# Kernel tuning notes

Hardware: AMD Instinct MI355X
Metric: run time of the kernel (lower is better)

The kernel has to match this reference:

```python
import jax, jax.numpy as jnp
import numpy as np

N_RULES = 64  # R
OUT_PER_RULE = 64  # O, fc out = R*O = 4096


def setup_inputs() -> dict:
    key = jax.random.key(0)
    k1, k2, k3, k4 = jax.random.split(key, 4)
    S, D_IN = 8192, 1024
    RO = N_RULES * OUT_PER_RULE
    X = jax.random.normal(k1, (S, D_IN), dtype=jnp.float32)
    # torch.nn.Linear-style weight [out, in] and bias [out]
    W = jax.random.normal(k2, (RO, D_IN), dtype=jnp.float32) * (1.0 / np.sqrt(D_IN))
    b = jax.random.normal(k3, (RO,), dtype=jnp.float32) * 0.01
    # rule firing strengths (computed under no_grad in the original)
    lambdas = jax.random.uniform(k4, (S, N_RULES), dtype=jnp.float32)
    return {"X": X, "W": W, "b": b, "lambdas": lambdas}


def reference(X, W, b, lambdas):
    # fc + sigmoid: [S, R*O]
    H = jax.nn.sigmoid(X @ W.T + b)
    S = H.shape[0]
    # apply_rule_strength: block-diagonal lambda_eye @ H^T is exactly a
    # rule-weighted sum over the R consecutive O-sized blocks of H.
    Hr = H.reshape(S, N_RULES, OUT_PER_RULE)  # [S, R, O]
    Y = jnp.einsum("sr,sro->so", lambdas, Hr)  # [S, O]
    return Y
```

## Files before the change

kernel.cpp:

```cpp
#include <hip/hip_runtime.h>

#define S_DIM 8192
#define K_DIM 1024
#define RO_DIM 4096
#define O_DIM 64
#define SO (S_DIM * O_DIM)
#define NSLICE 16

typedef __attribute__((ext_vector_type(8))) __bf16 bf16x8;
typedef __attribute__((ext_vector_type(4))) float floatx4;
typedef __attribute__((ext_vector_type(4))) unsigned short ushx4;
typedef __attribute__((ext_vector_type(8))) unsigned short ushx8;

__device__ inline unsigned short f2bf(float f) {
  unsigned u = __builtin_bit_cast(unsigned, f);
  u += 0x7fff + ((u >> 16) & 1);
  return (unsigned short)(u >> 16);
}
__device__ inline float bf2f(unsigned short h) {
  unsigned u = ((unsigned)h) << 16;
  return __builtin_bit_cast(float, u);
}

__global__ __launch_bounds__(256) void cast_kernel(const float* __restrict__ X,
                                                   const float* __restrict__ W,
                                                   unsigned short* __restrict__ Xb,
                                                   unsigned short* __restrict__ Wb) {
  const int NX4 = (S_DIM * K_DIM) / 4;
#pragma unroll
  for (int i = 0; i < 4; ++i) {
    int g = blockIdx.x * 1024 + i * 256 + threadIdx.x;
    float4 v;
    unsigned short* dst;
    if (g < NX4) {
      v = ((const float4*)X)[g];
      dst = Xb + (size_t)g * 4;
    } else {
      int j = g - NX4;
      v = ((const float4*)W)[j];
      dst = Wb + (size_t)j * 4;
    }
    ushx4 o;
    o.x = f2bf(v.x); o.y = f2bf(v.y); o.z = f2bf(v.z); o.w = f2bf(v.w);
    *(ushx4*)dst = o;
  }
}


template <int MB, int NB>
__device__ __forceinline__ void mfmaq(floatx4 (&acc)[8][4], const bf16x8 (&afr)[4][2],
                                      const bf16x8 (&bfr)[4][2]) {
  __builtin_amdgcn_s_setprio(1);
#pragma unroll
  for (int m = 0; m < 4; ++m)
#pragma unroll
    for (int n = 0; n < 2; ++n) {
      acc[MB + m][NB + n] = __builtin_amdgcn_mfma_f32_16x16x32_bf16(
          afr[m][0], bfr[NB + n][0], acc[MB + m][NB + n], 0, 0, 0);
      acc[MB + m][NB + n] = __builtin_amdgcn_mfma_f32_16x16x32_bf16(
          afr[m][1], bfr[NB + n][1], acc[MB + m][NB + n], 0, 0, 0);
    }
  __builtin_amdgcn_s_setprio(0);
}

#define BAR() __builtin_amdgcn_s_barrier()
#define LGKM0() asm volatile("s_waitcnt lgkmcnt(0)" ::: "memory")
#define SB0() __builtin_amdgcn_sched_barrier(0)

__global__ __launch_bounds__(512, 2) void gemm_kernel(const unsigned short* __restrict__ Xb,
                                                      const unsigned short* __restrict__ Wb,
                                                      const float* __restrict__ bias,
                                                      const float* __restrict__ lam,
                                                      unsigned short* __restrict__ partial) {
  __shared__ __align__(16) unsigned char smem[135168];
  unsigned short* sm = (unsigned short*)smem;
  float* lamsh = (float*)(smem + 131072);

  const int t = threadIdx.x;
  const int lane = t & 63;
  const int w = t >> 6;
  const int wm = w >> 2;
  const int wn = w & 3;
  const int quad = lane >> 4;
  const int l16 = lane & 15;

  int id = blockIdx.y * 16 + blockIdx.x;
  int x = id & 7;
  int j = id >> 3;
  const int bx = 2 * x + (j & 1);
  const int by = j >> 1;
  const int gm0 = by * 256;
  const int gn0 = bx * 256;

  const int rowt = t >> 3;
  const int gcc = (t & 7) ^ (rowt & 7);
  const size_t goff = (size_t)rowt * K_DIM + (size_t)gcc * 8;
  const unsigned short* Abase = Xb + (size_t)gm0 * K_DIM;
  const unsigned short* Bbase = Wb + (size_t)gn0 * K_DIM;

  auto STAGE = [&](const unsigned short* gbase, int half, int ktile, int slotOff) {
#pragma unroll
    for (int jj = 0; jj < 2; ++jj) {
      const unsigned short* src =
          gbase + (size_t)(half * 128 + jj * 64) * K_DIM + ktile * 64 + goff;
      __builtin_amdgcn_global_load_lds(
          (const __attribute__((address_space(1))) void*)src,
          (__attribute__((address_space(3))) void*)(sm + slotOff + jj * 4096 + t * 8),
          16, 0, 0);
    }
  };

  STAGE(Abase, 0, 0, 0);
  STAGE(Abase, 1, 0, 8192);
  STAGE(Bbase, 0, 0, 16384);
  STAGE(Bbase, 1, 0, 24576);
  STAGE(Bbase, 0, 1, 32768 + 16384);
  STAGE(Bbase, 1, 1, 32768 + 24576);
  STAGE(Abase, 0, 1, 32768 + 0);

  {
    int i = t;
    lamsh[i] = lam[(size_t)(gm0 + (i >> 2)) * 64 + bx * 4 + (i & 3)];
    i = t + 512;
    lamsh[i] = lam[(size_t)(gm0 + (i >> 2)) * 64 + bx * 4 + (i & 3)];
  }
  asm volatile("s_waitcnt vmcnt(6)" ::: "memory");
  BAR();

  floatx4 acc[8][4];
#pragma unroll
  for (int ni = 0; ni < 4; ++ni) {
    float bv = bias[gn0 + wn * 64 + ni * 16 + l16];
#pragma unroll
    for (int mi = 0; mi < 8; ++mi) acc[mi][ni] = (floatx4){bv, bv, bv, bv};
  }

  const int cA0 = ((quad) ^ (l16 & 7)) * 8;
  const int cA1 = ((4 + quad) ^ (l16 & 7)) * 8;

  for (int kt = 0; kt < 16; ++kt) {
    const int b = kt & 1;
    const unsigned short* As = sm + b * 32768 + wm * 8192 + l16 * 64;
    const unsigned short* Bs = sm + b * 32768 + 16384 + wn * 4096 + l16 * 64;
    const int bufN = (b ^ 1) * 32768;
    const int bufC = b * 32768;

    bf16x8 afr[4][2], bfr[4][2];

#pragma unroll
    for (int m = 0; m < 4; ++m) {
      afr[m][0] = *(const bf16x8*)(As + m * 1024 + cA0);
      afr[m][1] = *(const bf16x8*)(As + m * 1024 + cA1);
    }
#pragma unroll
    for (int n = 0; n < 2; ++n) {
      bfr[n][0] = *(const bf16x8*)(Bs + n * 1024 + cA0);
      bfr[n][1] = *(const bf16x8*)(Bs + n * 1024 + cA1);
    }
    if (kt < 15) STAGE(Abase, 1, kt + 1, bufN + 8192);
    BAR();
    LGKM0();
    SB0();
    mfmaq<0, 0>(acc, afr, bfr);
    BAR();

#pragma unroll
    for (int n = 2; n < 4; ++n) {
      bfr[n][0] = *(const bf16x8*)(Bs + n * 1024 + cA0);
      bfr[n][1] = *(const bf16x8*)(Bs + n * 1024 + cA1);
    }
    BAR();
    LGKM0();
    SB0();
    mfmaq<0, 2>(acc, afr, bfr);
    BAR();

#pragma unroll
    for (int m = 0; m < 4; ++m) {
      afr[m][0] = *(const bf16x8*)(As + (4 + m) * 1024 + cA0);
      afr[m][1] = *(const bf16x8*)(As + (4 + m) * 1024 + cA1);
    }
    if (kt < 14) STAGE(Bbase, 0, kt + 2, bufC + 16384);
    BAR();
    LGKM0();
    SB0();
    mfmaq<4, 0>(acc, afr, bfr);
    BAR();

    if (kt < 14) {
      STAGE(Bbase, 1, kt + 2, bufC + 24576);
      STAGE(Abase, 0, kt + 2, bufC + 0);
    }
    SB0();
    mfmaq<4, 2>(acc, afr, bfr);
    SB0();
    if (kt < 14) {
      asm volatile("s_waitcnt vmcnt(6)" ::: "memory");
    } else if (kt == 14) {
      asm volatile("s_waitcnt vmcnt(0)" ::: "memory");
    }
    BAR();
  }

  __syncthreads();
  {
    unsigned short* yreg = sm + wn * 16384;
#pragma unroll
    for (int mi = 0; mi < 8; ++mi) {
#pragma unroll
      for (int r = 0; r < 4; ++r) {
        int row = wm * 128 + mi * 16 + quad * 4 + r;
        float lamv = lamsh[row * 4 + wn];
#pragma unroll
        for (int ni = 0; ni < 4; ++ni) {
          float sg = 1.f / (1.f + __expf(-acc[mi][ni][r]));
          yreg[row * 64 + ((ni ^ quad) * 16) + l16] = f2bf(lamv * sg);
        }
      }
    }
  }
  __syncthreads();
  {
    unsigned short* pb = partial + (size_t)bx * SO + (size_t)gm0 * 64;
#pragma unroll
    for (int g = 0; g < 4; ++g) {
      int idx = g * 4096 + t * 8;
      int row = idx >> 6;
      int c = idx & 63;
      int phys = row * 64 + ((((c >> 4) ^ ((row >> 2) & 3))) << 4) + (c & 15);
      float s[8];
#pragma unroll
      for (int jj = 0; jj < 8; ++jj) s[jj] = 0.f;
#pragma unroll
      for (int q = 0; q < 4; ++q) {
        ushx8 v = *(const ushx8*)(sm + q * 16384 + phys);
#pragma unroll
        for (int jj = 0; jj < 8; ++jj) s[jj] += bf2f(v[jj]);
      }
      ushx8 o;
#pragma unroll
      for (int jj = 0; jj < 8; ++jj) o[jj] = f2bf(s[jj]);
      *(ushx8*)(pb + idx) = o;
    }
  }
}

__global__ __launch_bounds__(256) void reduce_kernel(const unsigned short* __restrict__ partial,
                                                     float* __restrict__ Y) {
  int i4 = blockIdx.x * 256 + threadIdx.x;
  float s0 = 0.f, s1 = 0.f, s2 = 0.f, s3 = 0.f;
#pragma unroll
  for (int c = 0; c < NSLICE; ++c) {
    ushx4 v = ((const ushx4*)(partial + (size_t)c * SO))[i4];
    s0 += bf2f(v.x); s1 += bf2f(v.y); s2 += bf2f(v.z); s3 += bf2f(v.w);
  }
  ((float4*)Y)[i4] = (float4){s0, s1, s2, s3};
}

extern "C" void kernel_launch(void* const* d_in, const int* in_sizes, int n_in,
                              void* d_out, int out_size, void* d_ws, size_t ws_size,
                              hipStream_t stream) {
  const float* X = (const float*)d_in[0];
  const float* W = (const float*)d_in[1];
  const float* b = (const float*)d_in[2];
  const float* lam = (const float*)d_in[3];
  float* Y = (float*)d_out;

  unsigned short* Xb = (unsigned short*)d_ws;
  unsigned short* Wb = Xb + (size_t)S_DIM * K_DIM;
  unsigned short* partial = Wb + (size_t)RO_DIM * K_DIM;

  int nCast = ((S_DIM + RO_DIM) * K_DIM / 4) / 1024;
  cast_kernel<<<nCast, 256, 0, stream>>>(X, W, Xb, Wb);

  dim3 g(RO_DIM / 256, S_DIM / 256);
  gemm_kernel<<<g, 512, 0, stream>>>(Xb, Wb, b, lam, partial);

  reduce_kernel<<<SO / 1024, 256, 0, stream>>>(partial, Y);
}
```

Baseline: 167.3 us.

## Fuse cast, GEMM, and reduce into one cooperative persistent kernel

Replaces the three launches (bf16 cast, tiled GEMM with sigmoid and lambda epilogue, slice reduce) with one cooperative kernel of 256 blocks. The stages are separated by grid-wide syncs, and each block handles two M tiles in sequence. The aim is to remove per-launch overhead and the inter-kernel gaps. In exchange it adds two grid barriers, and the 256 resident blocks (2 per CU) may get less latency hiding and tail balancing than the original 512-block GEMM grid.

New measurement: 435.8 us. 160% more time.

```diff
diff --git a/kernel.cpp b/kernel.cpp
--- a/kernel.cpp
+++ b/kernel.cpp
@@ -1,4 +1,7 @@
 #include <hip/hip_runtime.h>
+#include <hip/hip_cooperative_groups.h>
+
+namespace cg = cooperative_groups;
 
 #define S_DIM 8192
 #define K_DIM 1024
@@ -22,31 +25,6 @@
   return __builtin_bit_cast(float, u);
 }
 
-__global__ __launch_bounds__(256) void cast_kernel(const float* __restrict__ X,
-                                                   const float* __restrict__ W,
-                                                   unsigned short* __restrict__ Xb,
-                                                   unsigned short* __restrict__ Wb) {
-  const int NX4 = (S_DIM * K_DIM) / 4;
-#pragma unroll
-  for (int i = 0; i < 4; ++i) {
-    int g = blockIdx.x * 1024 + i * 256 + threadIdx.x;
-    float4 v;
-    unsigned short* dst;
-    if (g < NX4) {
-      v = ((const float4*)X)[g];
-      dst = Xb + (size_t)g * 4;
-    } else {
-      int j = g - NX4;
-      v = ((const float4*)W)[j];
-      dst = Wb + (size_t)j * 4;
-    }
-    ushx4 o;
-    o.x = f2bf(v.x); o.y = f2bf(v.y); o.z = f2bf(v.z); o.w = f2bf(v.w);
-    *(ushx4*)dst = o;
-  }
-}
-
-
 template <int MB, int NB>
 __device__ __forceinline__ void mfmaq(floatx4 (&acc)[8][4], const bf16x8 (&afr)[4][2],
                                       const bf16x8 (&bfr)[4][2]) {
@@ -67,16 +45,46 @@
 #define LGKM0() asm volatile("s_waitcnt lgkmcnt(0)" ::: "memory")
 #define SB0() __builtin_amdgcn_sched_barrier(0)
 
-__global__ __launch_bounds__(512, 2) void gemm_kernel(const unsigned short* __restrict__ Xb,
-                                                      const unsigned short* __restrict__ Wb,
-                                                      const float* __restrict__ bias,
-                                                      const float* __restrict__ lam,
-                                                      unsigned short* __restrict__ partial) {
+__global__ __launch_bounds__(512, 2) void fused_kernel(const float* __restrict__ X,
+                                                       const float* __restrict__ W,
+                                                       const float* __restrict__ bias,
+                                                       const float* __restrict__ lam,
+                                                       unsigned short* __restrict__ Xb,
+                                                       unsigned short* __restrict__ Wb,
+                                                       unsigned short* __restrict__ partial,
+                                                       float* __restrict__ Y) {
   __shared__ __align__(16) unsigned char smem[135168];
   unsigned short* sm = (unsigned short*)smem;
   float* lamsh = (float*)(smem + 131072);
 
+  cg::grid_group grid = cg::this_grid();
+
   const int t = threadIdx.x;
+
+  {
+    const int NX4 = (S_DIM * K_DIM) / 4;
+    const int NT4 = NX4 + (RO_DIM * K_DIM) / 4;
+    int g = blockIdx.x * 512 + t;
+#pragma unroll 4
+    for (int it = 0; it < 24; ++it, g += 131072) {
+      float4 v;
+      unsigned short* dst;
+      if (g < NX4) {
+        v = ((const float4*)X)[g];
+        dst = Xb + (size_t)g * 4;
+      } else {
+        int jx = g - NX4;
+        v = ((const float4*)W)[jx];
+        dst = Wb + (size_t)jx * 4;
+      }
+      ushx4 o;
+      o.x = f2bf(v.x); o.y = f2bf(v.y); o.z = f2bf(v.z); o.w = f2bf(v.w);
+      *(ushx4*)dst = o;
+    }
+  }
+  __threadfence();
+  grid.sync();
+
   const int lane = t & 63;
   const int w = t >> 6;
   const int wm = w >> 2;
@@ -84,177 +92,185 @@
   const int quad = lane >> 4;
   const int l16 = lane & 15;
 
-  int id = blockIdx.y * 16 + blockIdx.x;
-  int x = id & 7;
-  int j = id >> 3;
+  const int id = blockIdx.x;
+  const int x = id & 7;
+  const int j = id >> 3;
   const int bx = 2 * x + (j & 1);
-  const int by = j >> 1;
-  const int gm0 = by * 256;
+  const int by0 = j >> 1;
   const int gn0 = bx * 256;
 
   const int rowt = t >> 3;
   const int gcc = (t & 7) ^ (rowt & 7);
   const size_t goff = (size_t)rowt * K_DIM + (size_t)gcc * 8;
-  const unsigned short* Abase = Xb + (size_t)gm0 * K_DIM;
   const unsigned short* Bbase = Wb + (size_t)gn0 * K_DIM;
-
-  auto STAGE = [&](const unsigned short* gbase, int half, int ktile, int slotOff) {
-#pragma unroll
-    for (int jj = 0; jj < 2; ++jj) {
-      const unsigned short* src =
-          gbase + (size_t)(half * 128 + jj * 64) * K_DIM + ktile * 64 + goff;
-      __builtin_amdgcn_global_load_lds(
-          (const __attribute__((address_space(1))) void*)src,
-          (__attribute__((address_space(3))) void*)(sm + slotOff + jj * 4096 + t * 8),
-          16, 0, 0);
-    }
-  };
-
-  STAGE(Abase, 0, 0, 0);
-  STAGE(Abase, 1, 0, 8192);
-  STAGE(Bbase, 0, 0, 16384);
-  STAGE(Bbase, 1, 0, 24576);
-  STAGE(Bbase, 0, 1, 32768 + 16384);
-  STAGE(Bbase, 1, 1, 32768 + 24576);
-  STAGE(Abase, 0, 1, 32768 + 0);
-
-  {
-    int i = t;
-    lamsh[i] = lam[(size_t)(gm0 + (i >> 2)) * 64 + bx * 4 + (i & 3)];
-    i = t + 512;
-    lamsh[i] = lam[(size_t)(gm0 + (i >> 2)) * 64 + bx * 4 + (i & 3)];
-  }
-  asm volatile("s_waitcnt vmcnt(6)" ::: "memory");
-  BAR();
-
-  floatx4 acc[8][4];
-#pragma unroll
-  for (int ni = 0; ni < 4; ++ni) {
-    float bv = bias[gn0 + wn * 64 + ni * 16 + l16];
-#pragma unroll
-    for (int mi = 0; mi < 8; ++mi) acc[mi][ni] = (floatx4){bv, bv, bv, bv};
-  }
 
   const int cA0 = ((quad) ^ (l16 & 7)) * 8;
   const int cA1 = ((4 + quad) ^ (l16 & 7)) * 8;
 
-  for (int kt = 0; kt < 16; ++kt) {
-    const int b = kt & 1;
-    const unsigned short* As = sm + b * 32768 + wm * 8192 + l16 * 64;
-    const unsigned short* Bs = sm + b * 32768 + 16384 + wn * 4096 + l16 * 64;
-    const int bufN = (b ^ 1) * 32768;
-    const int bufC = b * 32768;
-
-    bf16x8 afr[4][2], bfr[4][2];
-
-#pragma unroll
-    for (int m = 0; m < 4; ++m) {
-      afr[m][0] = *(const bf16x8*)(As + m * 1024 + cA0);
-      afr[m][1] = *(const bf16x8*)(As + m * 1024 + cA1);
-    }
-#pragma unroll
-    for (int n = 0; n < 2; ++n) {
-      bfr[n][0] = *(const bf16x8*)(Bs + n * 1024 + cA0);
-      bfr[n][1] = *(const bf16x8*)(Bs + n * 1024 + cA1);
-    }
-    if (kt < 15) STAGE(Abase, 1, kt + 1, bufN + 8192);
+  for (int rep = 0; rep < 2; ++rep) {
+    const int by = by0 + rep * 16;
+    const int gm0 = by * 256;
+    const unsigned short* Abase = Xb + (size_t)gm0 * K_DIM;
+
+    auto STAGE = [&](const unsigned short* gbase, int half, int ktile, int slotOff) {
+#pragma unroll
+      for (int jj = 0; jj < 2; ++jj) {
+        const unsigned short* src =
+            gbase + (size_t)(half * 128 + jj * 64) * K_DIM + ktile * 64 + goff;
+        __builtin_amdgcn_global_load_lds(
+            (const __attribute__((address_space(1))) void*)src,
+            (__attribute__((address_space(3))) void*)(sm + slotOff + jj * 4096 + t * 8),
+            16, 0, 0);
+      }
+    };
+
+    __syncthreads();
+
+    STAGE(Abase, 0, 0, 0);
+    STAGE(Abase, 1, 0, 8192);
+    STAGE(Bbase, 0, 0, 16384);
+    STAGE(Bbase, 1, 0, 24576);
+    STAGE(Bbase, 0, 1, 32768 + 16384);
+    STAGE(Bbase, 1, 1, 32768 + 24576);
+    STAGE(Abase, 0, 1, 32768 + 0);
+
+    {
+      int i = t;
+      lamsh[i] = lam[(size_t)(gm0 + (i >> 2)) * 64 + bx * 4 + (i & 3)];
+      i = t + 512;
+      lamsh[i] = lam[(size_t)(gm0 + (i >> 2)) * 64 + bx * 4 + (i & 3)];
+    }
+    asm volatile("s_waitcnt vmcnt(6)" ::: "memory");
     BAR();
-    LGKM0();
-    SB0();
-    mfmaq<0, 0>(acc, afr, bfr);
-    BAR();
-
-#pragma unroll
-    for (int n = 2; n < 4; ++n) {
-      bfr[n][0] = *(const bf16x8*)(Bs + n * 1024 + cA0);
-      bfr[n][1] = *(const bf16x8*)(Bs + n * 1024 + cA1);
-    }
-    BAR();
-    LGKM0();
-    SB0();
-    mfmaq<0, 2>(acc, afr, bfr);
-    BAR();
-
-#pragma unroll
-    for (int m = 0; m < 4; ++m) {
-      afr[m][0] = *(const bf16x8*)(As + (4 + m) * 1024 + cA0);
-      afr[m][1] = *(const bf16x8*)(As + (4 + m) * 1024 + cA1);
-    }
-    if (kt < 14) STAGE(Bbase, 0, kt + 2, bufC + 16384);
-    BAR();
-    LGKM0();
-    SB0();
-    mfmaq<4, 0>(acc, afr, bfr);
-    BAR();
-
-    if (kt < 14) {
-      STAGE(Bbase, 1, kt + 2, bufC + 24576);
-      STAGE(Abase, 0, kt + 2, bufC + 0);
-    }
-    SB0();
-    mfmaq<4, 2>(acc, afr, bfr);
-    SB0();
-    if (kt < 14) {
-      asm volatile("s_waitcnt vmcnt(6)" ::: "memory");
-    } else if (kt == 14) {
-      asm volatile("s_waitcnt vmcnt(0)" ::: "memory");
-    }
-    BAR();
+
+    floatx4 acc[8][4];
+#pragma unroll
+    for (int ni = 0; ni < 4; ++ni) {
+      float bv = bias[gn0 + wn * 64 + ni * 16 + l16];
+#pragma unroll
+      for (int mi = 0; mi < 8; ++mi) acc[mi][ni] = (floatx4){bv, bv, bv, bv};
+    }
+
+    for (int kt = 0; kt < 16; ++kt) {
+      const int b = kt & 1;
+      const unsigned short* As = sm + b * 32768 + wm * 8192 + l16 * 64;
+      const unsigned short* Bs = sm + b * 32768 + 16384 + wn * 4096 + l16 * 64;
+      const int bufN = (b ^ 1) * 32768;
+      const int bufC = b * 32768;
+
+      bf16x8 afr[4][2], bfr[4][2];
+
+#pragma unroll
+      for (int m = 0; m < 4; ++m) {
+        afr[m][0] = *(const bf16x8*)(As + m * 1024 + cA0);
+        afr[m][1] = *(const bf16x8*)(As + m * 1024 + cA1);
+      }
+#pragma unroll
+      for (int n = 0; n < 2; ++n) {
+        bfr[n][0] = *(const bf16x8*)(Bs + n * 1024 + cA0);
+        bfr[n][1] = *(const bf16x8*)(Bs + n * 1024 + cA1);
+      }
+      if (kt < 15) STAGE(Abase, 1, kt + 1, bufN + 8192);
+      BAR();
+      LGKM0();
+      SB0();
+      mfmaq<0, 0>(acc, afr, bfr);
+      BAR();
+
+#pragma unroll
+      for (int n = 2; n < 4; ++n) {
+        bfr[n][0] = *(const bf16x8*)(Bs + n * 1024 + cA0);
+        bfr[n][1] = *(const bf16x8*)(Bs + n * 1024 + cA1);
+      }
+      BAR();
+      LGKM0();
+      SB0();
+      mfmaq<0, 2>(acc, afr, bfr);
+      BAR();
+
+#pragma unroll
+      for (int m = 0; m < 4; ++m) {
+        afr[m][0] = *(const bf16x8*)(As + (4 + m) * 1024 + cA0);
+        afr[m][1] = *(const bf16x8*)(As + (4 + m) * 1024 + cA1);
+      }
+      if (kt < 14) STAGE(Bbase, 0, kt + 2, bufC + 16384);
+      BAR();
+      LGKM0();
+      SB0();
+      mfmaq<4, 0>(acc, afr, bfr);
+      BAR();
+
+      if (kt < 14) {
+        STAGE(Bbase, 1, kt + 2, bufC + 24576);
+        STAGE(Abase, 0, kt + 2, bufC + 0);
+      }
+      SB0();
+      mfmaq<4, 2>(acc, afr, bfr);
+      SB0();
+      if (kt < 14) {
+        asm volatile("s_waitcnt vmcnt(6)" ::: "memory");
+      } else if (kt == 14) {
+        asm volatile("s_waitcnt vmcnt(0)" ::: "memory");
+      }
+      BAR();
+    }
+
+    __syncthreads();
+    {
+      unsigned short* yreg = sm + wn * 16384;
+#pragma unroll
+      for (int mi = 0; mi < 8; ++mi) {
+#pragma unroll
+        for (int r = 0; r < 4; ++r) {
+          int row = wm * 128 + mi * 16 + quad * 4 + r;
+          float lamv = lamsh[row * 4 + wn];
+#pragma unroll
+          for (int ni = 0; ni < 4; ++ni) {
+            float sg = 1.f / (1.f + __expf(-acc[mi][ni][r]));
+            yreg[row * 64 + ((ni ^ quad) * 16) + l16] = f2bf(lamv * sg);
+          }
+        }
+      }
+    }
+    __syncthreads();
+    {
+      unsigned short* pb = partial + (size_t)bx * SO + (size_t)gm0 * 64;
+#pragma unroll
+      for (int g = 0; g < 4; ++g) {
+        int idx = g * 4096 + t * 8;
+        int row = idx >> 6;
+        int c = idx & 63;
+        int phys = row * 64 + ((((c >> 4) ^ ((row >> 2) & 3))) << 4) + (c & 15);
+        float s[8];
+#pragma unroll
+        for (int jj = 0; jj < 8; ++jj) s[jj] = 0.f;
+#pragma unroll
+        for (int q = 0; q < 4; ++q) {
+          ushx8 v = *(const ushx8*)(sm + q * 16384 + phys);
+#pragma unroll
+          for (int jj = 0; jj < 8; ++jj) s[jj] += bf2f(v[jj]);
+        }
+        ushx8 o;
+#pragma unroll
+        for (int jj = 0; jj < 8; ++jj) o[jj] = f2bf(s[jj]);
+        *(ushx8*)(pb + idx) = o;
+      }
+    }
   }
 
-  __syncthreads();
+  __threadfence();
+  grid.sync();
+
   {
-    unsigned short* yreg = sm + wn * 16384;
-#pragma unroll
-    for (int mi = 0; mi < 8; ++mi) {
-#pragma unroll
-      for (int r = 0; r < 4; ++r) {
-        int row = wm * 128 + mi * 16 + quad * 4 + r;
-        float lamv = lamsh[row * 4 + wn];
-#pragma unroll
-        for (int ni = 0; ni < 4; ++ni) {
-          float sg = 1.f / (1.f + __expf(-acc[mi][ni][r]));
-          yreg[row * 64 + ((ni ^ quad) * 16) + l16] = f2bf(lamv * sg);
-        }
-      }
-    }
+    int i4 = blockIdx.x * 512 + t;
+    float s0 = 0.f, s1 = 0.f, s2 = 0.f, s3 = 0.f;
+#pragma unroll
+    for (int c = 0; c < NSLICE; ++c) {
+      ushx4 v = ((const ushx4*)(partial + (size_t)c * SO))[i4];
+      s0 += bf2f(v.x); s1 += bf2f(v.y); s2 += bf2f(v.z); s3 += bf2f(v.w);
+    }
+    ((float4*)Y)[i4] = (float4){s0, s1, s2, s3};
   }
-  __syncthreads();
-  {
-    unsigned short* pb = partial + (size_t)bx * SO + (size_t)gm0 * 64;
-#pragma unroll
-    for (int g = 0; g < 4; ++g) {
-      int idx = g * 4096 + t * 8;
-      int row = idx >> 6;
-      int c = idx & 63;
-      int phys = row * 64 + ((((c >> 4) ^ ((row >> 2) & 3))) << 4) + (c & 15);
-      float s[8];
-#pragma unroll
-      for (int jj = 0; jj < 8; ++jj) s[jj] = 0.f;
-#pragma unroll
-      for (int q = 0; q < 4; ++q) {
-        ushx8 v = *(const ushx8*)(sm + q * 16384 + phys);
-#pragma unroll
-        for (int jj = 0; jj < 8; ++jj) s[jj] += bf2f(v[jj]);
-      }
-      ushx8 o;
-#pragma unroll
-      for (int jj = 0; jj < 8; ++jj) o[jj] = f2bf(s[jj]);
-      *(ushx8*)(pb + idx) = o;
-    }
-  }
-}
-
-__global__ __launch_bounds__(256) void reduce_kernel(const unsigned short* __restrict__ partial,
-                                                     float* __restrict__ Y) {
-  int i4 = blockIdx.x * 256 + threadIdx.x;
-  float s0 = 0.f, s1 = 0.f, s2 = 0.f, s3 = 0.f;
-#pragma unroll
-  for (int c = 0; c < NSLICE; ++c) {
-    ushx4 v = ((const ushx4*)(partial + (size_t)c * SO))[i4];
-    s0 += bf2f(v.x); s1 += bf2f(v.y); s2 += bf2f(v.z); s3 += bf2f(v.w);
-  }
-  ((float4*)Y)[i4] = (float4){s0, s1, s2, s3};
 }
 
 extern "C" void kernel_launch(void* const* d_in, const int* in_sizes, int n_in,
@@ -270,11 +286,8 @@
   unsigned short* Wb = Xb + (size_t)S_DIM * K_DIM;
   unsigned short* partial = Wb + (size_t)RO_DIM * K_DIM;
 
-  int nCast = ((S_DIM + RO_DIM) * K_DIM / 4) / 1024;
-  cast_kernel<<<nCast, 256, 0, stream>>>(X, W, Xb, Wb);
-
-  dim3 g(RO_DIM / 256, S_DIM / 256);
-  gemm_kernel<<<g, 512, 0, stream>>>(Xb, Wb, b, lam, partial);
-
-  reduce_kernel<<<SO / 1024, 256, 0, stream>>>(partial, Y);
-}
+  void* args[] = {(void*)&X, (void*)&W, (void*)&b, (void*)&lam,
+                  (void*)&Xb, (void*)&Wb, (void*)&partial, (void*)&Y};
+  hipLaunchCooperativeKernel((const void*)fused_kernel, dim3(256), dim3(512),
+                             args, 0, stream);
+}
```
